# Performance work log

Measured on AMD Instinct MI355X. Metric: run time of the kernel, lower is better.

## Reference

```python
import jax, jax.numpy as jnp
import numpy as np

NR = 116  # number of AAL ROIs
VOL = (61, 73, 61)
V = 61 * 73 * 61


def setup_inputs() -> dict:
    B, C, D, T = 8, 192, 2, 24  # batch MUST be 8: fc1 outputs 64 = B*B
    key = jax.random.key(0)
    ks = jax.random.split(key, 16)
    s = 0.02
    # synthetic AAL template: every voxel gets a ROI label 0..115, all present
    rng = np.random.default_rng(0)
    labels_np = rng.integers(0, NR, size=V).astype(np.int32)
    labels_np[:NR] = np.arange(NR)
    # ROI centroid pairwise distances (compute_node_distances equivalent)
    coords = np.stack(np.meshgrid(np.arange(61), np.arange(73), np.arange(61), indexing='ij'), -1).reshape(V, 3).astype(np.float64)
    cent = np.zeros((NR, 3))
    for r in range(NR):
        cent[r] = coords[labels_np == r].mean(0)
    dist = np.linalg.norm(cent[:, None] - cent[None, :], axis=-1).astype(np.float32)
    return {
        'x': jax.random.normal(ks[0], (B, C, D, D, D, T), jnp.float32),
        'roi_labels': jnp.asarray(labels_np.reshape(VOL)),
        'node_distances': jnp.asarray(dist),
        'fc_w': s * jax.random.normal(ks[1], (V, C * D * D * D), jnp.float32),
        'fc_b': jnp.zeros((V,), jnp.float32),
        'fs_w1': s * jax.random.normal(ks[2], (NR, 64), jnp.float32),
        'fs_b1': jnp.zeros((NR, 64), jnp.float32),
        'fs_w2': s * jax.random.normal(ks[3], (NR, 64, 64), jnp.float32),
        'fs_b2': jnp.zeros((NR, 64), jnp.float32),
        'fs_w3': s * jax.random.normal(ks[4], (NR, 64), jnp.float32),
        'fs_b3': jnp.zeros((NR,), jnp.float32),
        'm_w1': s * jax.random.normal(ks[5], (64,), jnp.float32),
        'm_b1': jnp.zeros((64,), jnp.float32),
        'm_w2': s * jax.random.normal(ks[6], (64, 64), jnp.float32),
        'm_b2': jnp.zeros((64,), jnp.float32),
        'm_w3': s * jax.random.normal(ks[7], (64,), jnp.float32),
        'm_b3': jnp.zeros((1,), jnp.float32),
        'fc1_w': s * jax.random.normal(ks[8], (64, NR * NR), jnp.float32),
        'fc1_b': jnp.zeros((64,), jnp.float32),
        'hidden_w': s * jax.random.normal(ks[9], (768, 192 + NR), jnp.float32),
        'hidden_b': jnp.zeros((768,), jnp.float32),
        'out_w': s * jax.random.normal(ks[10], (1, 768), jnp.float32),
        'out_b': jnp.zeros((1,), jnp.float32),
    }


def _forward(x, node_distances, fc_w, fc_b, fs_w1, fs_b1, fs_w2, fs_b2, fs_w3, fs_b3,
             m_w1, m_b1, m_w2, m_b2, m_w3, m_b3, fc1_w, fc1_b,
             hidden_w, hidden_b, out_w, out_b, labels):
    B, T = x.shape[0], x.shape[-1]
    # fc projects each time frame into the 61x73x61 volume: [B,T,V]
    xt = jnp.swapaxes(x.reshape(B, -1, T), 1, 2)            # [B,T,1536]
    vox = jnp.einsum('bti,vi->btv', xt, fc_w) + fc_b        # [B,T,V]
    # ROI time series = segment-mean of voxels per ROI (replaces python loops)
    seg = jax.ops.segment_sum(jnp.moveaxis(vox, 2, 0).reshape(V, B * T), labels, num_segments=NR)
    cnt = jax.ops.segment_sum(jnp.ones((V,), vox.dtype), labels, num_segments=NR)
    ts = (seg / jnp.maximum(cnt, 1.0)[:, None]).reshape(NR, B, T)
    x_node = ts.mean(axis=2).T                              # [B,116]
    # 116 tiny per-ROI MLPs, vectorized (eval mode: dropout is identity)
    h = jax.nn.relu(x_node[..., None] * fs_w1[None] + fs_b1[None])       # [B,116,64]
    h = jax.nn.relu(jnp.einsum('bni,noi->bno', h, fs_w2) + fs_b2[None])  # [B,116,64]
    fx = jnp.einsum('bni,ni->bn', h, fs_w3) + fs_b3[None]                # [B,116]
    # distance MLP m over all 116*116 pairwise distances
    d = node_distances.reshape(-1, 1)                       # [13456,1]
    g = jax.nn.relu(d * m_w1[None, :] + m_b1)
    g = jax.nn.relu(g @ m_w2.T + m_b2)
    md = (g @ m_w3[:, None] + m_b3).reshape(-1)             # [13456]
    mmat = (fc1_w @ md + fc1_b).reshape(B, B)               # requires B*B == 64
    mf = mmat @ fx                                          # [B,116]
    # avgpool branch: mean over all spatial*time positions -> [B,192]
    pooled = x.reshape(B, x.shape[1], -1).mean(axis=2)
    cat = jnp.concatenate([mf, pooled], axis=1)             # [B,308]
    hid = cat @ hidden_w.T + hidden_b                       # no activation (as in source)
    return hid @ out_w.T + out_b                            # [B,1]


def reference(x, roi_labels, node_distances, fc_w, fc_b, fs_w1, fs_b1, fs_w2, fs_b2, fs_w3, fs_b3,
              m_w1, m_b1, m_w2, m_b2, m_w3, m_b3, fc1_w, fc1_b, hidden_w, hidden_b, out_w, out_b):
    return _forward(x, node_distances, fc_w, fc_b, fs_w1, fs_b1, fs_w2, fs_b2, fs_w3, fs_b3,
                    m_w1, m_b1, m_w2, m_b2, m_w3, m_b3, fc1_w, fc1_b,
                    hidden_w, hidden_b, out_w, out_b, roi_labels.reshape(-1))
```

## Files before the change

### kernel.cpp

```cpp
#include <hip/hip_runtime.h>

#define V_TOT 271633
#define NRR 116
#define CIN 1536
#define T_LEN 24
#define B_SZ 8
#define NP (NRR*NRR)
#define CATN 308
#define SPLITS 44
#define NST (NRR*SPLITS)
#define VB 1062
#define WPAD 310
#define DPS 12
#define DISTB 2243
#define SMALLN (DISTB + 8)
#define GROUPS 464
#define MEGA_GRID (GROUPS * 16)

typedef float nfloat4 __attribute__((ext_vector_type(4)));

__global__ __launch_bounds__(256) void hist_xbar_kernel(const int* __restrict__ labels,
                                                        int* __restrict__ blockHist,
                                                        const float* __restrict__ x,
                                                        float* __restrict__ xbar) {
    if (blockIdx.x < VB) {
        __shared__ int h[NRR];
        for (int i = threadIdx.x; i < NRR; i += 256) h[i] = 0;
        __syncthreads();
        int v = blockIdx.x * 256 + threadIdx.x;
        if (v < V_TOT) atomicAdd(&h[labels[v]], 1);
        __syncthreads();
        for (int i = threadIdx.x; i < NRR; i += 256)
            blockHist[(size_t)i * VB + blockIdx.x] = h[i];
    } else {
        int idx = (blockIdx.x - VB) * 256 + threadIdx.x;
        if (idx < B_SZ * CIN) {
            const float* p = x + (size_t)idx * T_LEN;
            float s = 0.f;
            #pragma unroll
            for (int t = 0; t < T_LEN; ++t) s += p[t];
            xbar[idx] = s * (1.0f / T_LEN);
        }
    }
}

__global__ __launch_bounds__(256) void binscan_kernel(const int* __restrict__ blockHist,
                                                      int* __restrict__ blockBase,
                                                      int* __restrict__ counts) {
    const int r = blockIdx.x;
    const int lane = threadIdx.x & 63, w = threadIdx.x >> 6;
    __shared__ int wsum[4];
    int run = 0;
    for (int base = 0; base < VB; base += 256) {
        const int i = base + threadIdx.x;
        const int orig = (i < VB) ? blockHist[(size_t)r * VB + i] : 0;
        int val = orig;
        #pragma unroll
        for (int off = 1; off < 64; off <<= 1) {
            int t = __shfl_up(val, off);
            if (lane >= off) val += t;
        }
        if (lane == 63) wsum[w] = val;
        __syncthreads();
        int woff = 0;
        #pragma unroll
        for (int j = 0; j < 4; ++j) if (j < w) woff += wsum[j];
        if (i < VB) blockBase[(size_t)r * VB + i] = run + woff + val - orig;
        int tot = wsum[0] + wsum[1] + wsum[2] + wsum[3];
        __syncthreads();
        run += tot;
    }
    if (threadIdx.x == 0) counts[r] = run;
}

__device__ __forceinline__ void roi_off(const int* __restrict__ counts, int r,
                                        int& off, int& n) {
    const int lane = threadIdx.x & 63;
    int a = counts[lane];
    int b = (lane + 64 < NRR) ? counts[lane + 64] : 0;
    int sa = a, sb = b;
    #pragma unroll
    for (int d = 1; d < 64; d <<= 1) {
        int t = __shfl_up(sa, d); if (lane >= d) sa += t;
        t = __shfl_up(sb, d);     if (lane >= d) sb += t;
    }
    const int tot_a = __shfl(sa, 63);
    if (r == 0) off = 0;
    else if (r < 64) off = __shfl(sa, r - 1);
    else if (r == 64) off = tot_a;
    else off = tot_a + __shfl(sb, r - 65);
    n = counts[r];
}

__global__ __launch_bounds__(256) void scatter_kernel(const int* __restrict__ labels,
                                                      const int* __restrict__ counts,
                                                      const int* __restrict__ blockBase,
                                                      int* __restrict__ perm) {
    __shared__ int lab[256];
    __shared__ int offs_s[NRR];
    const int v = blockIdx.x * 256 + threadIdx.x;
    const int r = (v < V_TOT) ? labels[v] : -1;
    lab[threadIdx.x] = r;
    if (threadIdx.x < 64) {
        const int lane = threadIdx.x;
        int a = counts[lane];
        int b = (lane + 64 < NRR) ? counts[lane + 64] : 0;
        int sa = a, sb = b;
        #pragma unroll
        for (int d = 1; d < 64; d <<= 1) {
            int t = __shfl_up(sa, d); if (lane >= d) sa += t;
            t = __shfl_up(sb, d);     if (lane >= d) sb += t;
        }
        const int tot_a = __shfl(sa, 63);
        offs_s[lane] = sa - a;
        if (lane + 64 < NRR) offs_s[lane + 64] = tot_a + sb - b;
    }
    __syncthreads();
    if (r >= 0) {
        int rank = 0;
        for (int t = 0; t < (int)threadIdx.x; ++t) rank += (lab[t] == r);
        perm[offs_s[r] + blockBase[(size_t)r * VB + blockIdx.x] + rank] = v;
    }
}

__device__ __forceinline__ void add4(float4& a, const float4 b) {
    a.x += b.x; a.y += b.y; a.z += b.z; a.w += b.w;
}
__device__ __forceinline__ float4 ldnt4(const float* p) {
    nfloat4 v = __builtin_nontemporal_load((const nfloat4*)p);
    return make_float4(v.x, v.y, v.z, v.w);
}

__global__ __launch_bounds__(384, 6) void mega_kernel(
        const float* __restrict__ fc_w, const float* __restrict__ fc_b,
        const int* __restrict__ perm, const int* __restrict__ counts,
        const float* __restrict__ xbar, float* __restrict__ dotpart,
        const float* __restrict__ dist,
        const float* __restrict__ mw1, const float* __restrict__ mb1,
        const float* __restrict__ mw2, const float* __restrict__ mb2,
        const float* __restrict__ mw3, const float* __restrict__ mb3,
        float* __restrict__ md,
        const float* __restrict__ hidden_w, const float* __restrict__ hidden_b,
        const float* __restrict__ out_w, const float* __restrict__ out_b,
        float* __restrict__ weffpart) {
    const int g = blockIdx.x >> 4, m = blockIdx.x & 15;
    const int lane = threadIdx.x & 63, w = threadIdx.x >> 6;

    if (m >= 11) {
        const int idx = g * 5 + (m - 11);
        if (idx >= SMALLN) return;
        if (idx < DISTB) {
            const int p = idx * 6 + w;
            if (p < NP) {
                float d = dist[p];
                float g1 = fmaxf(d * mw1[lane] + mb1[lane], 0.f);
                const float* w2row = mw2 + lane * 64;
                float acc = mb2[lane];
                #pragma unroll
                for (int i = 0; i < 64; ++i) acc += __shfl(g1, i) * w2row[i];
                float g2 = fmaxf(acc, 0.f);
                float t = g2 * mw3[lane];
                for (int s = 32; s > 0; s >>= 1) t += __shfl_down(t, s);
                if (lane == 0) md[p] = t + mb3[0];
            }
        } else {
            const int jb = idx - DISTB;
            const int k = threadIdx.x;
            const int j0 = jb * 96, j1 = j0 + 96;
            if (k < CATN) {
                float s = 0.f;
                for (int j = j0; j < j1; ++j) s += hidden_w[(size_t)j * CATN + k] * out_w[j];
                weffpart[jb*WPAD + k] = s;
            } else if (k == CATN) {
                float s = 0.f;
                for (int j = j0; j < j1; ++j) s += hidden_b[j] * out_w[j];
                weffpart[jb*WPAD + CATN] = s + (jb == 0 ? out_b[0] : 0.f);
            }
        }
        return;
    }

    const int sbid = g * 11 + m;
    const int r = sbid / SPLITS, s = sbid % SPLITS;
    int off, n;
    roi_off(counts, r, off, n);
    const int chunk = (n + SPLITS - 1) / SPLITS;
    const int k0 = min(s * chunk, n);
    const int k1 = min(k0 + chunk, n);
    const int c4 = threadIdx.x * 4;

    float4 a0{0,0,0,0}, a1{0,0,0,0}, a2{0,0,0,0}, a3{0,0,0,0};
    float4 a4{0,0,0,0}, a5{0,0,0,0}, a6{0,0,0,0}, a7{0,0,0,0};
    int k = k0;
    for (; k + 8 <= k1; k += 8) {
        const int v0 = perm[off+k+0], v1 = perm[off+k+1], v2 = perm[off+k+2], v3 = perm[off+k+3];
        const int v4 = perm[off+k+4], v5 = perm[off+k+5], v6 = perm[off+k+6], v7 = perm[off+k+7];
        const float4 x0 = ldnt4(fc_w + (size_t)v0*CIN + c4);
        const float4 x1 = ldnt4(fc_w + (size_t)v1*CIN + c4);
        const float4 x2 = ldnt4(fc_w + (size_t)v2*CIN + c4);
        const float4 x3 = ldnt4(fc_w + (size_t)v3*CIN + c4);
        const float4 x4 = ldnt4(fc_w + (size_t)v4*CIN + c4);
        const float4 x5 = ldnt4(fc_w + (size_t)v5*CIN + c4);
        const float4 x6 = ldnt4(fc_w + (size_t)v6*CIN + c4);
        const float4 x7 = ldnt4(fc_w + (size_t)v7*CIN + c4);
        add4(a0, x0); add4(a1, x1); add4(a2, x2); add4(a3, x3);
        add4(a4, x4); add4(a5, x5); add4(a6, x6); add4(a7, x7);
    }
    for (; k < k1; ++k) {
        const int v = perm[off+k];
        add4(a0, ldnt4(fc_w + (size_t)v*CIN + c4));
    }
    add4(a0, a1); add4(a2, a3); add4(a4, a5); add4(a6, a7);
    add4(a0, a2); add4(a4, a6); add4(a0, a4);

    float bacc = 0.f;
    for (int kk = k0 + threadIdx.x; kk < k1; kk += 384) bacc += fc_b[perm[off+kk]];

    float d[B_SZ];
    #pragma unroll
    for (int b = 0; b < B_SZ; ++b) {
        const float4 xb = *(const float4*)(xbar + b*CIN + c4);
        d[b] = a0.x*xb.x + a0.y*xb.y + a0.z*xb.z + a0.w*xb.w;
    }
    __shared__ float red[6][9];
    #pragma unroll
    for (int b = 0; b < B_SZ; ++b) {
        float v = d[b];
        for (int sft = 32; sft > 0; sft >>= 1) v += __shfl_down(v, sft);
        if (lane == 0) red[w][b] = v;
    }
    {
        float v = bacc;
        for (int sft = 32; sft > 0; sft >>= 1) v += __shfl_down(v, sft);
        if (lane == 0) red[w][8] = v;
    }
    __syncthreads();
    if (threadIdx.x < 9) {
        float v = 0.f;
        #pragma unroll
        for (int j = 0; j < 6; ++j) v += red[j][threadIdx.x];
        dotpart[((size_t)(r*SPLITS + s))*DPS + threadIdx.x] = v;
    }
}

__global__ __launch_bounds__(256) void mid_kernel(
        const float* __restrict__ dotpart, const int* __restrict__ counts,
        const float* __restrict__ w1, const float* __restrict__ b1,
        const float* __restrict__ w2, const float* __restrict__ b2,
        const float* __restrict__ w3, const float* __restrict__ b3,
        float* __restrict__ fx,
        const float* __restrict__ fc1_w, const float* __restrict__ md,
        float* __restrict__ mmatpart) {
    const int bid = blockIdx.x;
    const int lane = threadIdx.x & 63;
    if (bid < 232) {
        int w = bid * 4 + (threadIdx.x >> 6);
        int b = w / NRR, r = w % NRR;
        float sdot = 0.f, sb = 0.f;
        if (lane < SPLITS) {
            const float* p = dotpart + ((size_t)(r*SPLITS + lane))*DPS;
            sdot = p[b]; sb = p[8];
        }
        #pragma unroll
        for (int off = 32; off > 0; off >>= 1) {
            sdot += __shfl_xor(sdot, off);
            sb   += __shfl_xor(sb, off);
        }
        float xn = (sdot + sb) / (float)counts[r];

        float h1 = fmaxf(xn * w1[r*64 + lane] + b1[r*64 + lane], 0.f);
        const float* w2row = w2 + ((size_t)r*64 + lane) * 64;
        float acc = b2[r*64 + lane];
        #pragma unroll
        for (int i = 0; i < 64; ++i) acc += __shfl(h1, i) * w2row[i];
        float h2 = fmaxf(acc, 0.f);
        float p = h2 * w3[r*64 + lane];
        for (int sft = 32; sft > 0; sft >>= 1) p += __shfl_down(p, sft);
        if (lane == 0) fx[b * NRR + r] = p + b3[r];
    } else {
        const int fb = bid - 232;
        const int j = fb >> 2, q = fb & 3;
        const int p0 = q * (NP/4), p1 = p0 + (NP/4);
        const float* row = fc1_w + (size_t)j * NP;
        float s = 0.f;
        for (int p = p0 + threadIdx.x; p < p1; p += 256) s += row[p] * md[p];
        __shared__ float red[4];
        for (int sft = 32; sft > 0; sft >>= 1) s += __shfl_down(s, sft);
        if ((threadIdx.x & 63) == 0) red[threadIdx.x >> 6] = s;
        __syncthreads();
        if (threadIdx.x == 0) mmatpart[j*4 + q] = red[0] + red[1] + red[2] + red[3];
    }
}

__global__ __launch_bounds__(512) void tail_kernel(const float* __restrict__ mmatpart,
                                                   const float* __restrict__ fc1_b,
                                                   const float* __restrict__ fx,
                                                   const float* __restrict__ xbar,
                                                   const float* __restrict__ weffpart,
                                                   float* __restrict__ out) {
    __shared__ float mmat[64];
    __shared__ float cat[B_SZ][CATN];
    if (threadIdx.x < 64) {
        const float* p = mmatpart + threadIdx.x*4;
        mmat[threadIdx.x] = p[0] + p[1] + p[2] + p[3] + fc1_b[threadIdx.x];
    }
    __syncthreads();
    for (int idx = threadIdx.x; idx < B_SZ * NRR; idx += 512) {
        int b = idx / NRR, r = idx % NRR;
        float s = 0.f;
        #pragma unroll
        for (int kk = 0; kk < 8; ++kk) s += mmat[b*8 + kk] * fx[kk * NRR + r];
        cat[b][r] = s;
    }
    for (int idx = threadIdx.x; idx < B_SZ * 192; idx += 512) {
        int b = idx / 192, c = idx % 192;
        float s = 0.f;
        #pragma unroll
        for (int j = 0; j < 8; ++j) s += xbar[b * CIN + c*8 + j];
        cat[b][NRR + c] = s * (1.0f / 8.0f);
    }
    __syncthreads();
    const int b = threadIdx.x >> 6, lane = threadIdx.x & 63;
    float s = 0.f;
    for (int k = lane; k < CATN; k += 64) {
        float wk = 0.f;
        #pragma unroll
        for (int jb = 0; jb < 8; ++jb) wk += weffpart[jb*WPAD + k];
        s += cat[b][k] * wk;
    }
    for (int sft = 32; sft > 0; sft >>= 1) s += __shfl_down(s, sft);
    if (lane == 0) {
        float beff = 0.f;
        #pragma unroll
        for (int jb = 0; jb < 8; ++jb) beff += weffpart[jb*WPAD + CATN];
        out[b] = s + beff;
    }
}

extern "C" void kernel_launch(void* const* d_in, const int* in_sizes, int n_in,
                              void* d_out, int out_size, void* d_ws, size_t ws_size,
                              hipStream_t stream) {
    const float* x        = (const float*)d_in[0];
    const int*   labels   = (const int*)d_in[1];
    const float* dist     = (const float*)d_in[2];
    const float* fc_w     = (const float*)d_in[3];
    const float* fc_b     = (const float*)d_in[4];
    const float* fs_w1    = (const float*)d_in[5];
    const float* fs_b1    = (const float*)d_in[6];
    const float* fs_w2    = (const float*)d_in[7];
    const float* fs_b2    = (const float*)d_in[8];
    const float* fs_w3    = (const float*)d_in[9];
    const float* fs_b3    = (const float*)d_in[10];
    const float* m_w1     = (const float*)d_in[11];
    const float* m_b1     = (const float*)d_in[12];
    const float* m_w2     = (const float*)d_in[13];
    const float* m_b2     = (const float*)d_in[14];
    const float* m_w3     = (const float*)d_in[15];
    const float* m_b3     = (const float*)d_in[16];
    const float* fc1_w    = (const float*)d_in[17];
    const float* fc1_b    = (const float*)d_in[18];
    const float* hidden_w = (const float*)d_in[19];
    const float* hidden_b = (const float*)d_in[20];
    const float* out_w    = (const float*)d_in[21];
    const float* out_b    = (const float*)d_in[22];
    float* out = (float*)d_out;

    int* counts    = (int*)d_ws;
    int* blockHist = counts + 128;
    int* blockBase = blockHist + NRR*VB;
    int* perm      = blockBase + NRR*VB;
    float* fb = (float*)(perm + ((V_TOT + 255) / 256) * 256);
    float* dotpart  = fb;  fb += (size_t)NRR * SPLITS * DPS;
    float* xbar     = fb;  fb += B_SZ * CIN;
    float* fx       = fb;  fb += B_SZ * NRR + 32;
    float* md       = fb;  fb += NP;
    float* mmatpart = fb;  fb += 256;
    float* weffpart = fb;  fb += 8 * WPAD;

    hist_xbar_kernel<<<VB + 48, 256, 0, stream>>>(labels, blockHist, x, xbar);
    binscan_kernel<<<NRR, 256, 0, stream>>>(blockHist, blockBase, counts);
    scatter_kernel<<<VB, 256, 0, stream>>>(labels, counts, blockBase, perm);
    mega_kernel<<<MEGA_GRID, 384, 0, stream>>>(
        fc_w, fc_b, perm, counts, xbar, dotpart,
        dist, m_w1, m_b1, m_w2, m_b2, m_w3, m_b3, md,
        hidden_w, hidden_b, out_w, out_b, weffpart);
    mid_kernel<<<488, 256, 0, stream>>>(dotpart, counts,
        fs_w1, fs_b1, fs_w2, fs_b2, fs_w3, fs_b3, fx, fc1_w, md, mmatpart);
    tail_kernel<<<1, 512, 0, stream>>>(mmatpart, fc1_b, fx, xbar, weffpart, out);
}
```

Measured before the change: 368.4 us.

## Move distance MLP and weff work into pre kernel; warp-ballot scatter ranking

Moves the per-pair distance MLP and the hidden/out weight folding out of the bandwidth-bound mega kernel into the first preprocessing kernel. The mega kernel then launches only its fc_w-streaming blocks, with no interleaved small-work blocks. The scatter kernel replaces its O(256) serial shared-memory rank loop with a 64-step wavefront shuffle count plus a per-wave histogram in shared memory. The cost is that the MLP work now runs serially before the scan rather than overlapping with the weight streaming.

Measured after the change: 343.4 us. 1.07x faster.

```diff
diff --git a/kernel.cpp b/kernel.cpp
--- a/kernel.cpp
+++ b/kernel.cpp
@@ -12,28 +12,57 @@
 #define VB 1062
 #define WPAD 310
 #define DPS 12
-#define DISTB 2243
-#define SMALLN (DISTB + 8)
-#define GROUPS 464
-#define MEGA_GRID (GROUPS * 16)
+
+#define DISTB4 3364
+#define PRE_HIST0 DISTB4
+#define PRE_XBAR0 (DISTB4 + VB)
+#define PRE_WEFF0 (DISTB4 + VB + 48)
+#define PRE_GRID  (PRE_WEFF0 + 16)
 
 typedef float nfloat4 __attribute__((ext_vector_type(4)));
 
-__global__ __launch_bounds__(256) void hist_xbar_kernel(const int* __restrict__ labels,
-                                                        int* __restrict__ blockHist,
-                                                        const float* __restrict__ x,
-                                                        float* __restrict__ xbar) {
-    if (blockIdx.x < VB) {
-        __shared__ int h[NRR];
+__global__ __launch_bounds__(256) void pre_kernel(
+        const int* __restrict__ labels, int* __restrict__ blockHist,
+        const float* __restrict__ x, float* __restrict__ xbar,
+        const float* __restrict__ dist,
+        const float* __restrict__ mw1, const float* __restrict__ mb1,
+        const float* __restrict__ mw2, const float* __restrict__ mb2,
+        const float* __restrict__ mw3, const float* __restrict__ mb3,
+        float* __restrict__ md,
+        const float* __restrict__ hidden_w, const float* __restrict__ hidden_b,
+        const float* __restrict__ out_w, const float* __restrict__ out_b,
+        float* __restrict__ weffpart) {
+    __shared__ int h[NRR];
+    const int bid = blockIdx.x;
+    const int lane = threadIdx.x & 63, w = threadIdx.x >> 6;
+
+    if (bid < DISTB4) {
+        const int p = bid * 4 + w;
+        float d = dist[p];
+        float g1 = fmaxf(d * mw1[lane] + mb1[lane], 0.f);
+        const float* w2row = mw2 + lane * 64;
+        float acc = mb2[lane];
+        #pragma unroll
+        for (int i = 0; i < 64; ++i) acc += __shfl(g1, i) * w2row[i];
+        float g2 = fmaxf(acc, 0.f);
+        float t = g2 * mw3[lane];
+        for (int s = 32; s > 0; s >>= 1) t += __shfl_down(t, s);
+        if (lane == 0) md[p] = t + mb3[0];
+        return;
+    }
+    if (bid < PRE_XBAR0) {
+        const int hb = bid - PRE_HIST0;
         for (int i = threadIdx.x; i < NRR; i += 256) h[i] = 0;
         __syncthreads();
-        int v = blockIdx.x * 256 + threadIdx.x;
+        int v = hb * 256 + threadIdx.x;
         if (v < V_TOT) atomicAdd(&h[labels[v]], 1);
         __syncthreads();
         for (int i = threadIdx.x; i < NRR; i += 256)
-            blockHist[(size_t)i * VB + blockIdx.x] = h[i];
-    } else {
-        int idx = (blockIdx.x - VB) * 256 + threadIdx.x;
+            blockHist[(size_t)i * VB + hb] = h[i];
+        return;
+    }
+    if (bid < PRE_WEFF0) {
+        int idx = (bid - PRE_XBAR0) * 256 + threadIdx.x;
         if (idx < B_SZ * CIN) {
             const float* p = x + (size_t)idx * T_LEN;
             float s = 0.f;
@@ -41,6 +70,20 @@
             for (int t = 0; t < T_LEN; ++t) s += p[t];
             xbar[idx] = s * (1.0f / T_LEN);
         }
+        return;
+    }
+    const int idx = bid - PRE_WEFF0;
+    const int jb = idx >> 1, kb = idx & 1;
+    const int k = kb * 256 + threadIdx.x;
+    const int j0 = jb * 96, j1 = j0 + 96;
+    if (k < CATN) {
+        float s = 0.f;
+        for (int j = j0; j < j1; ++j) s += hidden_w[(size_t)j * CATN + k] * out_w[j];
+        weffpart[jb*WPAD + k] = s;
+    } else if (k == CATN) {
+        float s = 0.f;
+        for (int j = j0; j < j1; ++j) s += hidden_b[j] * out_w[j];
+        weffpart[jb*WPAD + CATN] = s + (jb == 0 ? out_b[0] : 0.f);
     }
 }
 
@@ -96,15 +139,15 @@
                                                       const int* __restrict__ counts,
                                                       const int* __restrict__ blockBase,
                                                       int* __restrict__ perm) {
-    __shared__ int lab[256];
     __shared__ int offs_s[NRR];
-    const int v = blockIdx.x * 256 + threadIdx.x;
+    __shared__ int wh[4][NRR];
+    const int tid = threadIdx.x, lane = tid & 63, w = tid >> 6;
+    const int v = blockIdx.x * 256 + tid;
     const int r = (v < V_TOT) ? labels[v] : -1;
-    lab[threadIdx.x] = r;
-    if (threadIdx.x < 64) {
-        const int lane = threadIdx.x;
-        int a = counts[lane];
-        int b = (lane + 64 < NRR) ? counts[lane + 64] : 0;
+    for (int i = tid; i < 4*NRR; i += 256) ((int*)wh)[i] = 0;
+    if (tid < 64) {
+        int a = counts[tid];
+        int b = (tid + 64 < NRR) ? counts[tid + 64] : 0;
         int sa = a, sb = b;
         #pragma unroll
         for (int d = 1; d < 64; d <<= 1) {
@@ -112,14 +155,23 @@
             t = __shfl_up(sb, d);     if (lane >= d) sb += t;
         }
         const int tot_a = __shfl(sa, 63);
-        offs_s[lane] = sa - a;
-        if (lane + 64 < NRR) offs_s[lane + 64] = tot_a + sb - b;
-    }
+        offs_s[tid] = sa - a;
+        if (tid + 64 < NRR) offs_s[tid + 64] = tot_a + sb - b;
+    }
+    __syncthreads();
+    int rank = 0, cnt = 0;
+    #pragma unroll
+    for (int i = 0; i < 64; ++i) {
+        int ri = __shfl(r, i);
+        if (r >= 0 && ri == r) { cnt++; if (i < lane) rank++; }
+    }
+    if (r >= 0 && rank == 0) wh[w][r] = cnt;
     __syncthreads();
     if (r >= 0) {
-        int rank = 0;
-        for (int t = 0; t < (int)threadIdx.x; ++t) rank += (lab[t] == r);
-        perm[offs_s[r] + blockBase[(size_t)r * VB + blockIdx.x] + rank] = v;
+        int base = 0;
+        #pragma unroll
+        for (int w2 = 0; w2 < 3; ++w2) if (w2 < w) base += wh[w2][r];
+        perm[offs_s[r] + blockBase[(size_t)r * VB + blockIdx.x] + base + rank] = v;
     }
 }
 
@@ -134,53 +186,9 @@
 __global__ __launch_bounds__(384, 6) void mega_kernel(
         const float* __restrict__ fc_w, const float* __restrict__ fc_b,
         const int* __restrict__ perm, const int* __restrict__ counts,
-        const float* __restrict__ xbar, float* __restrict__ dotpart,
-        const float* __restrict__ dist,
-        const float* __restrict__ mw1, const float* __restrict__ mb1,
-        const float* __restrict__ mw2, const float* __restrict__ mb2,
-        const float* __restrict__ mw3, const float* __restrict__ mb3,
-        float* __restrict__ md,
-        const float* __restrict__ hidden_w, const float* __restrict__ hidden_b,
-        const float* __restrict__ out_w, const float* __restrict__ out_b,
-        float* __restrict__ weffpart) {
-    const int g = blockIdx.x >> 4, m = blockIdx.x & 15;
+        const float* __restrict__ xbar, float* __restrict__ dotpart) {
+    const int sbid = blockIdx.x;
     const int lane = threadIdx.x & 63, w = threadIdx.x >> 6;
-
-    if (m >= 11) {
-        const int idx = g * 5 + (m - 11);
-        if (idx >= SMALLN) return;
-        if (idx < DISTB) {
-            const int p = idx * 6 + w;
-            if (p < NP) {
-                float d = dist[p];
-                float g1 = fmaxf(d * mw1[lane] + mb1[lane], 0.f);
-                const float* w2row = mw2 + lane * 64;
-                float acc = mb2[lane];
-                #pragma unroll
-                for (int i = 0; i < 64; ++i) acc += __shfl(g1, i) * w2row[i];
-                float g2 = fmaxf(acc, 0.f);
-                float t = g2 * mw3[lane];
-                for (int s = 32; s > 0; s >>= 1) t += __shfl_down(t, s);
-                if (lane == 0) md[p] = t + mb3[0];
-            }
-        } else {
-            const int jb = idx - DISTB;
-            const int k = threadIdx.x;
-            const int j0 = jb * 96, j1 = j0 + 96;
-            if (k < CATN) {
-                float s = 0.f;
-                for (int j = j0; j < j1; ++j) s += hidden_w[(size_t)j * CATN + k] * out_w[j];
-                weffpart[jb*WPAD + k] = s;
-            } else if (k == CATN) {
-                float s = 0.f;
-                for (int j = j0; j < j1; ++j) s += hidden_b[j] * out_w[j];
-                weffpart[jb*WPAD + CATN] = s + (jb == 0 ? out_b[0] : 0.f);
-            }
-        }
-        return;
-    }
-
-    const int sbid = g * 11 + m;
     const int r = sbid / SPLITS, s = sbid % SPLITS;
     int off, n;
     roi_off(counts, r, off, n);
@@ -377,13 +385,13 @@
     float* mmatpart = fb;  fb += 256;
     float* weffpart = fb;  fb += 8 * WPAD;
 
-    hist_xbar_kernel<<<VB + 48, 256, 0, stream>>>(labels, blockHist, x, xbar);
+    pre_kernel<<<PRE_GRID, 256, 0, stream>>>(
+        labels, blockHist, x, xbar,
+        dist, m_w1, m_b1, m_w2, m_b2, m_w3, m_b3, md,
+        hidden_w, hidden_b, out_w, out_b, weffpart);
     binscan_kernel<<<NRR, 256, 0, stream>>>(blockHist, blockBase, counts);
     scatter_kernel<<<VB, 256, 0, stream>>>(labels, counts, blockBase, perm);
-    mega_kernel<<<MEGA_GRID, 384, 0, stream>>>(
-        fc_w, fc_b, perm, counts, xbar, dotpart,
-        dist, m_w1, m_b1, m_w2, m_b2, m_w3, m_b3, md,
-        hidden_w, hidden_b, out_w, out_b, weffpart);
+    mega_kernel<<<NST, 384, 0, stream>>>(fc_w, fc_b, perm, counts, xbar, dotpart);
     mid_kernel<<<488, 256, 0, stream>>>(dotpart, counts,
         fs_w1, fs_b1, fs_w2, fs_b2, fs_w3, fs_b3, fx, fc1_w, md, mmatpart);
     tail_kernel<<<1, 512, 0, stream>>>(mmatpart, fc1_b, fx, xbar, weffpart, out);
```
